# Optimization experiments

Measured on AMD Instinct MI355X. Metric: run time of the kernel, lower is better.

Reference implementation:

```python
import jax, jax.numpy as jnp
import numpy as np

E, TOPK, H, I = 8, 2, 2048, 5632
T = 4096


def setup_inputs() -> dict:
    key = jax.random.key(0)
    k1, k2, k3, k4 = jax.random.split(key, 4)
    hidden_states = jax.random.normal(k1, (T, H), dtype=jnp.float32)
    gate_w = jax.random.normal(k2, (E, H), dtype=jnp.float32) * (1.0 / np.sqrt(H))
    # fused gate+up projection: [E, 2*I, H]
    w13 = jax.random.normal(k3, (E, 2 * I, H), dtype=jnp.float32) * (1.0 / np.sqrt(H))
    # down projection: [E, H, I]
    w2 = jax.random.normal(k4, (E, H, I), dtype=jnp.float32) * (1.0 / np.sqrt(I))
    return {"hidden_states": hidden_states, "gate_w": gate_w, "w13": w13, "w2": w2, "top_k": TOPK}


def reference(hidden_states, gate_w, w13, w2, top_k):
    num_experts = gate_w.shape[0]
    inter = w2.shape[2]
    # router: fp32 gate logits -> softmax -> top-k -> renormalize (FusedMoE renormalize=True)
    logits = hidden_states.astype(jnp.float32) @ gate_w.T          # [T, E]
    probs = jax.nn.softmax(logits, axis=-1)
    vals, idx = jax.lax.top_k(probs, top_k)                        # [T, k]
    vals = vals / jnp.sum(vals, axis=-1, keepdims=True)
    # dense routing weight matrix [T, E] (zero outside top-k)
    dense_w = jnp.sum(jax.nn.one_hot(idx, num_experts, dtype=vals.dtype) * vals[..., None], axis=1)

    def body(acc, inputs):
        w13_e, w2_e, we = inputs                                   # [2I,H], [H,I], [T]
        gu = hidden_states @ w13_e.T                               # [T, 2I]
        g, u = gu[:, :inter], gu[:, inter:]
        h = jax.nn.silu(g) * u                                     # SwiGLU
        y = h @ w2_e.T                                             # [T, H]
        return acc + we[:, None] * y, None

    acc0 = jnp.zeros_like(hidden_states)
    out, _ = jax.lax.scan(body, acc0, (w13, w2, dense_w.T))
    return out
```

## Files before the change

### kernel.cpp

```cpp
#include <hip/hip_runtime.h>

#define T_TOK 4096
#define H_DIM 2048
#define I_DIM 5632
#define NE 8

typedef _Float16 f16;
typedef _Float16 f16x8 __attribute__((ext_vector_type(8)));
typedef float f32x4 __attribute__((ext_vector_type(4)));

#define OFF_META   0
#define OFF_BTOK   256
#define OFF_BW     (256 + 32768)
#define OFF_RE     (256 + 2 * 32768)
#define OFF_RW     (256 + 3 * 32768)
#define OFF_TP     (256 + 4 * 32768)
#define OFF_HSB    (256 + 5 * 32768)
#define OFF_WF     (OFF_HSB + (size_t)T_TOK * H_DIM * 2)

typedef const __attribute__((address_space(1))) unsigned int guint;
typedef __attribute__((address_space(3))) unsigned int luint;

__device__ __forceinline__ int swzk(int r, int bir) {
    return (bir & 15) | ((((bir >> 4) ^ r) & 7) << 4);
}

__global__ void cvt_w_kernel(const float* __restrict__ src, f16* __restrict__ dst, int n8) {
    int stride = gridDim.x * blockDim.x;
    for (int i = blockIdx.x * blockDim.x + threadIdx.x; i < n8; i += stride) {
        size_t b = (size_t)i * 8;
        float4 a = *(const float4*)(src + b);
        float4 c = *(const float4*)(src + b + 4);
        f16x8 v;
        v[0] = (f16)a.x; v[1] = (f16)a.y; v[2] = (f16)a.z; v[3] = (f16)a.w;
        v[4] = (f16)c.x; v[5] = (f16)c.y; v[6] = (f16)c.z; v[7] = (f16)c.w;
        *(f16x8*)(dst + b) = v;
    }
}

__global__ void prep_kernel(const float* __restrict__ w13, f16* __restrict__ w13f, int n8_w13,
                            int cvt13_b,
                            const float* __restrict__ hs, f16* __restrict__ hsb,
                            const float* __restrict__ gw,
                            int* __restrict__ re, float* __restrict__ rw,
                            int* __restrict__ counts) {
    int id = blockIdx.x;
    if (id < cvt13_b) {
        int stride = cvt13_b * 256;
        for (int i = id * 256 + threadIdx.x; i < n8_w13; i += stride) {
            size_t b = (size_t)i * 8;
            float4 a = *(const float4*)(w13 + b);
            float4 c = *(const float4*)(w13 + b + 4);
            f16x8 v;
            v[0] = (f16)a.x; v[1] = (f16)a.y; v[2] = (f16)a.z; v[3] = (f16)a.w;
            v[4] = (f16)c.x; v[5] = (f16)c.y; v[6] = (f16)c.z; v[7] = (f16)c.w;
            *(f16x8*)(w13f + b) = v;
        }
        return;
    }
    id -= cvt13_b;
    if (id < 1024) {
        const int n8 = T_TOK * H_DIM / 8;
        int stride = 1024 * 256;
        for (int i = id * 256 + threadIdx.x; i < n8; i += stride) {
            size_t b = (size_t)i * 8;
            float4 a = *(const float4*)(hs + b);
            float4 c = *(const float4*)(hs + b + 4);
            f16x8 v;
            v[0] = (f16)a.x; v[1] = (f16)a.y; v[2] = (f16)a.z; v[3] = (f16)a.w;
            v[4] = (f16)c.x; v[5] = (f16)c.y; v[6] = (f16)c.z; v[7] = (f16)c.w;
            *(f16x8*)(hsb + b) = v;
        }
        return;
    }
    id -= 1024;
    int lane = threadIdx.x & 63;
    int t = id * 4 + (threadIdx.x >> 6);
    float acc[NE];
#pragma unroll
    for (int e = 0; e < NE; ++e) acc[e] = 0.f;
    const float* x = hs + (size_t)t * H_DIM;
    for (int i = lane; i < H_DIM; i += 64) {
        float xv = x[i];
#pragma unroll
        for (int e = 0; e < NE; ++e) acc[e] += xv * gw[e * H_DIM + i];
    }
#pragma unroll
    for (int e = 0; e < NE; ++e)
        for (int off = 32; off > 0; off >>= 1) acc[e] += __shfl_xor(acc[e], off);
    if (lane == 0) {
        int i1 = 0; float l1 = acc[0];
#pragma unroll
        for (int e = 1; e < NE; ++e) if (acc[e] > l1) { l1 = acc[e]; i1 = e; }
        int i2 = -1; float l2 = -1e30f;
#pragma unroll
        for (int e = 0; e < NE; ++e) if (e != i1 && acc[e] > l2) { l2 = acc[e]; i2 = e; }
        float aa = __expf(l2 - l1);
        float s = 1.f / (1.f + aa);
        re[t * 2] = i1; re[t * 2 + 1] = i2;
        rw[t * 2] = s;  rw[t * 2 + 1] = aa * s;
        atomicAdd(&counts[i1], 1);
        atomicAdd(&counts[i2], 1);
    }
}

__global__ void scan_kernel(int* __restrict__ meta) {
    if (threadIdx.x == 0) {
        int s = 0;
        for (int e = 0; e < NE; ++e) { meta[8 + e] = s; meta[16 + e] = s; s += meta[e]; }
    }
}

__global__ void place_kernel(const int* __restrict__ re, const float* __restrict__ rw,
                             int* __restrict__ cursor, int* __restrict__ btok,
                             float* __restrict__ bwv, int* __restrict__ tpos) {
    int t = blockIdx.x * 256 + threadIdx.x;
    if (t >= T_TOK) return;
#pragma unroll
    for (int s = 0; s < 2; ++s) {
        int e = re[t * 2 + s];
        int p = atomicAdd(&cursor[e], 1);
        btok[p] = t;
        bwv[p] = rw[t * 2 + s];
        tpos[t * 2 + s] = p;
    }
}

__device__ __forceinline__ void decode_panel(int id, int npx, int e_arg,
                                             int& e, int& bx, int& by) {
    if (e_arg >= 0) { e = e_arg; bx = id >> 5; by = id & 31; return; }
    int sg  = id >> 8;
    int rem = id & 255;
    by = rem >> 3;
    int P = sg * 8 + (rem & 7);
    e = P / npx; bx = P % npx;
}

__global__ __launch_bounds__(256, 4) void gemm1_kernel(
    const f16* __restrict__ w13f, const f16* __restrict__ hsb, f16* __restrict__ hb,
    const int* __restrict__ counts, const int* __restrict__ offs,
    const int* __restrict__ btok,
    const float* __restrict__ w2src, f16* __restrict__ w2dst, int cvt_n8, int cvt_blocks,
    int e_arg, int global_h)
{
    if ((int)blockIdx.x < cvt_blocks) {
        int stride = cvt_blocks * 256;
        for (int i = blockIdx.x * 256 + threadIdx.x; i < cvt_n8; i += stride) {
            size_t b = (size_t)i * 8;
            float4 a = *(const float4*)(w2src + b);
            float4 c = *(const float4*)(w2src + b + 4);
            f16x8 v;
            v[0] = (f16)a.x; v[1] = (f16)a.y; v[2] = (f16)a.z; v[3] = (f16)a.w;
            v[4] = (f16)c.x; v[5] = (f16)c.y; v[6] = (f16)c.z; v[7] = (f16)c.w;
            *(f16x8*)(w2dst + b) = v;
        }
        return;
    }
    int e, bx, by;
    decode_panel((int)blockIdx.x - cvt_blocks, 88, e_arg, e, bx, by);
    const int n_e = counts[e];
    if (by * 128 >= n_e) return;
    const int boff = offs[e];
    const f16* We = (e_arg >= 0) ? w13f : (w13f + (size_t)e * (2 * I_DIM) * H_DIM);

    const int tid = threadIdx.x;
    const int lane = tid & 63;
    const int wid = tid >> 6;
    const int wm = wid >> 1, wn = wid & 1;
    const int l15 = lane & 15;

    __shared__ f16 As[128 * 64];
    __shared__ f16 Bs[128 * 64];

    const f16* gA[4]; const f16* gB[4]; int dstc[4];
#pragma unroll
    for (int i = 0; i < 4; ++i) {
        int c = i * 256 + tid;
        int r = c >> 3;
        dstc[i] = c * 16;
        int slot = ((c & 7) ^ (r & 7)) * 8;
        int idx = by * 128 + r;
        idx = idx < n_e ? idx : n_e - 1;
        gA[i] = hsb + (size_t)btok[boff + idx] * H_DIM + slot;
        int wrow = (r < 64) ? (bx * 64 + r) : (I_DIM + bx * 64 + (r - 64));
        gB[i] = We + (size_t)wrow * H_DIM + slot;
    }

    f32x4 ag[4][2], au[4][2];
#pragma unroll
    for (int m = 0; m < 4; ++m)
#pragma unroll
        for (int n = 0; n < 2; ++n) { ag[m][n] = (f32x4)0.f; au[m][n] = (f32x4)0.f; }

    const int NT = H_DIM / 64;

#pragma unroll 1
    for (int kt = 0; kt < NT; ++kt) {
        __syncthreads();
        const int k0 = kt * 64;
#pragma unroll
        for (int i = 0; i < 4; ++i) {
            __builtin_amdgcn_global_load_lds((guint*)(gA[i] + k0), (luint*)((char*)As + dstc[i]), 16, 0, 0);
            __builtin_amdgcn_global_load_lds((guint*)(gB[i] + k0), (luint*)((char*)Bs + dstc[i]), 16, 0, 0);
        }
        __syncthreads();
#pragma unroll
        for (int kh = 0; kh < 2; ++kh) {
            const int kb = kh * 64 + (lane >> 4) * 16;
            f16x8 a[4], bg[2], bu[2];
#pragma unroll
            for (int m = 0; m < 4; ++m) {
                int r = wm * 64 + m * 16 + l15;
                a[m] = *(const f16x8*)((const char*)As + r * 128 + swzk(r, kb));
            }
#pragma unroll
            for (int n = 0; n < 2; ++n) {
                int rg = wn * 32 + n * 16 + l15;
                bg[n] = *(const f16x8*)((const char*)Bs + rg * 128 + swzk(rg, kb));
                int ru = 64 + rg;
                bu[n] = *(const f16x8*)((const char*)Bs + ru * 128 + swzk(ru, kb));
            }
#pragma unroll
            for (int m = 0; m < 4; ++m)
#pragma unroll
                for (int n = 0; n < 2; ++n) {
                    ag[m][n] = __builtin_amdgcn_mfma_f32_16x16x32_f16(a[m], bg[n], ag[m][n], 0, 0, 0);
                    au[m][n] = __builtin_amdgcn_mfma_f32_16x16x32_f16(a[m], bu[n], au[m][n], 0, 0, 0);
                }
        }
    }

    const int hbase = (global_h ? boff : 0) + by * 128;
#pragma unroll
    for (int m = 0; m < 4; ++m) {
        int rl0 = wm * 64 + m * 16 + ((lane >> 4) << 2);
#pragma unroll
        for (int r = 0; r < 4; ++r) {
            int rl = rl0 + r;
            if (by * 128 + rl < n_e) {
#pragma unroll
                for (int n = 0; n < 2; ++n) {
                    float g = ag[m][n][r];
                    float u = au[m][n][r];
                    float h = g / (1.f + __expf(-g)) * u;
                    hb[(size_t)(hbase + rl) * I_DIM + bx * 64 + wn * 32 + n * 16 + l15] = (f16)h;
                }
            }
        }
    }
}

__global__ __launch_bounds__(256, 4) void gemm2_kernel(
    const f16* __restrict__ w2f, const f16* __restrict__ hb, f16* __restrict__ y,
    const int* __restrict__ counts, const int* __restrict__ offs,
    const int* __restrict__ btok, int e_arg, int global_h)
{
    int e, bx, by;
    decode_panel(blockIdx.x, 16, e_arg, e, bx, by);
    const int n_e = counts[e];
    if (by * 128 >= n_e) return;
    const int boff = offs[e];
    const f16* We = (e_arg >= 0) ? w2f : (w2f + (size_t)e * H_DIM * I_DIM);

    const int tid = threadIdx.x;
    const int lane = tid & 63;
    const int wid = tid >> 6;
    const int wm = wid >> 1, wn = wid & 1;
    const int l15 = lane & 15;

    __shared__ f16 As[128 * 64];
    __shared__ f16 Bs[128 * 64];

    const int hb0 = global_h ? boff : 0;
    const f16* gA[4]; const f16* gB[4]; int dstc[4];
#pragma unroll
    for (int i = 0; i < 4; ++i) {
        int c = i * 256 + tid;
        int r = c >> 3;
        dstc[i] = c * 16;
        int slot = ((c & 7) ^ (r & 7)) * 8;
        int idx = by * 128 + r;
        idx = idx < n_e ? idx : n_e - 1;
        gA[i] = hb + (size_t)(hb0 + idx) * I_DIM + slot;
        gB[i] = We + (size_t)(bx * 128 + r) * I_DIM + slot;
    }

    f32x4 acc[4][4];
#pragma unroll
    for (int m = 0; m < 4; ++m)
#pragma unroll
        for (int n = 0; n < 4; ++n) acc[m][n] = (f32x4)0.f;

    const int NT = I_DIM / 64;

#pragma unroll 1
    for (int kt = 0; kt < NT; ++kt) {
        __syncthreads();
        const int k0 = kt * 64;
#pragma unroll
        for (int i = 0; i < 4; ++i) {
            __builtin_amdgcn_global_load_lds((guint*)(gA[i] + k0), (luint*)((char*)As + dstc[i]), 16, 0, 0);
            __builtin_amdgcn_global_load_lds((guint*)(gB[i] + k0), (luint*)((char*)Bs + dstc[i]), 16, 0, 0);
        }
        __syncthreads();
#pragma unroll
        for (int kh = 0; kh < 2; ++kh) {
            const int kb = kh * 64 + (lane >> 4) * 16;
            f16x8 a[4], b[4];
#pragma unroll
            for (int m = 0; m < 4; ++m) {
                int r = wm * 64 + m * 16 + l15;
                a[m] = *(const f16x8*)((const char*)As + r * 128 + swzk(r, kb));
            }
#pragma unroll
            for (int n = 0; n < 4; ++n) {
                int r = wn * 64 + n * 16 + l15;
                b[n] = *(const f16x8*)((const char*)Bs + r * 128 + swzk(r, kb));
            }
#pragma unroll
            for (int m = 0; m < 4; ++m)
#pragma unroll
                for (int n = 0; n < 4; ++n)
                    acc[m][n] = __builtin_amdgcn_mfma_f32_16x16x32_f16(a[m], b[n], acc[m][n], 0, 0, 0);
        }
    }

#pragma unroll
    for (int m = 0; m < 4; ++m) {
        int rl0 = wm * 64 + m * 16 + ((lane >> 4) << 2);
#pragma unroll
        for (int r = 0; r < 4; ++r) {
            int rl = rl0 + r;
            if (by * 128 + rl < n_e) {
                int p = boff + by * 128 + rl;
#pragma unroll
                for (int n = 0; n < 4; ++n)
                    y[(size_t)p * H_DIM + bx * 128 + wn * 64 + n * 16 + l15] = (f16)acc[m][n][r];
            }
        }
    }
}

__global__ void reduce_kernel(const f16* __restrict__ y, const int* __restrict__ tpos,
                              const float* __restrict__ bwv, float* __restrict__ out) {
    int t = blockIdx.x;
    int p0 = tpos[t * 2], p1 = tpos[t * 2 + 1];
    float w0 = bwv[p0], w1 = bwv[p1];
    const f16x8* y0 = (const f16x8*)(y + (size_t)p0 * H_DIM);
    const f16x8* y1 = (const f16x8*)(y + (size_t)p1 * H_DIM);
    float4* o = (float4*)(out + (size_t)t * H_DIM);
    for (int i = threadIdx.x; i < H_DIM / 8; i += 256) {
        f16x8 a = y0[i], b = y1[i];
        float4 r0, r1;
        r0.x = w0 * (float)a[0] + w1 * (float)b[0];
        r0.y = w0 * (float)a[1] + w1 * (float)b[1];
        r0.z = w0 * (float)a[2] + w1 * (float)b[2];
        r0.w = w0 * (float)a[3] + w1 * (float)b[3];
        r1.x = w0 * (float)a[4] + w1 * (float)b[4];
        r1.y = w0 * (float)a[5] + w1 * (float)b[5];
        r1.z = w0 * (float)a[6] + w1 * (float)b[6];
        r1.w = w0 * (float)a[7] + w1 * (float)b[7];
        o[i * 2]     = r0;
        o[i * 2 + 1] = r1;
    }
}

extern "C" void kernel_launch(void* const* d_in, const int* in_sizes, int n_in,
                              void* d_out, int out_size, void* d_ws, size_t ws_size,
                              hipStream_t stream) {
    const float* hs  = (const float*)d_in[0];
    const float* gw  = (const float*)d_in[1];
    const float* w13 = (const float*)d_in[2];
    const float* w2  = (const float*)d_in[3];
    float* out = (float*)d_out;

    char* ws = (char*)d_ws;
    int*   meta = (int*)(ws + OFF_META);
    int*   btok = (int*)(ws + OFF_BTOK);
    float* bwv  = (float*)(ws + OFF_BW);
    int*   re   = (int*)(ws + OFF_RE);
    float* rw   = (float*)(ws + OFF_RW);
    int*   tpos = (int*)(ws + OFF_TP);
    f16*   hsb  = (f16*)(ws + OFF_HSB);

    hipMemsetAsync(meta, 0, 256, stream);

    const size_t w13_elems = (size_t)NE * 2 * I_DIM * H_DIM;
    const size_t w2_elems  = (size_t)NE * H_DIM * I_DIM;

    size_t o_w13f = OFF_WF;
    size_t o_w2f  = o_w13f + w13_elems * 2;
    size_t o_hb   = o_w2f + w2_elems * 2;
    size_t o_y    = o_hb + (size_t)2 * T_TOK * I_DIM * 2;
    size_t need_full = o_y + (size_t)2 * T_TOK * H_DIM * 2;

    size_t f_w13 = OFF_WF;
    size_t f_w2  = f_w13 + (size_t)2 * I_DIM * H_DIM * 2;
    size_t f_hb  = f_w2 + (size_t)H_DIM * I_DIM * 2;
    size_t f_y   = f_hb + (size_t)T_TOK * I_DIM * 2;

    if (ws_size >= need_full) {
        f16* w13f = (f16*)(ws + o_w13f);
        f16* w2f  = (f16*)(ws + o_w2f);
        f16* hb   = (f16*)(ws + o_hb);
        f16* y    = (f16*)(ws + o_y);
        prep_kernel<<<3072 + 1024 + 1024, 256, 0, stream>>>(
            w13, w13f, (int)(w13_elems / 8), 3072, hs, hsb, gw, re, rw, meta);
        scan_kernel<<<1, 64, 0, stream>>>(meta);
        place_kernel<<<T_TOK / 256, 256, 0, stream>>>(re, rw, meta + 16, btok, bwv, tpos);
        gemm1_kernel<<<2048 + 704 * 32, 256, 0, stream>>>(
            w13f, hsb, hb, meta, meta + 8, btok,
            w2, w2f, (int)(w2_elems / 8), 2048, -1, 1);
        gemm2_kernel<<<128 * 32, 256, 0, stream>>>(w2f, hb, y, meta, meta + 8, btok, -1, 1);
        reduce_kernel<<<T_TOK, 256, 0, stream>>>(y, tpos, bwv, out);
    } else {
        f16* w13f = (f16*)(ws + f_w13);
        f16* w2f  = (f16*)(ws + f_w2);
        f16* hb   = (f16*)(ws + f_hb);
        f16* y    = (f16*)(ws + f_y);
        prep_kernel<<<1024 + 1024, 256, 0, stream>>>(
            w13, (f16*)nullptr, 0, 0, hs, hsb, gw, re, rw, meta);
        scan_kernel<<<1, 64, 0, stream>>>(meta);
        place_kernel<<<T_TOK / 256, 256, 0, stream>>>(re, rw, meta + 16, btok, bwv, tpos);
        const size_t w13_slice = (size_t)2 * I_DIM * H_DIM;
        const size_t w2_slice  = (size_t)H_DIM * I_DIM;
        for (int e = 0; e < NE; ++e) {
            cvt_w_kernel<<<2048, 256, 0, stream>>>(w13 + e * w13_slice, w13f, (int)(w13_slice / 8));
            gemm1_kernel<<<2048 + 88 * 32, 256, 0, stream>>>(
                w13f, hsb, hb, meta, meta + 8, btok,
                w2 + e * w2_slice, w2f, (int)(w2_slice / 8), 2048, e, 0);
            gemm2_kernel<<<16 * 32, 256, 0, stream>>>(w2f, hb, y, meta, meta + 8, btok, e, 0);
        }
        reduce_kernel<<<T_TOK, 256, 0, stream>>>(y, tpos, bwv, out);
    }
}
```

Baseline: 1.127 ms.

## Use two-wave blocks with larger per-wave tiles in both MoE GEMMs

```diff
diff --git a/kernel.cpp b/kernel.cpp
--- a/kernel.cpp
+++ b/kernel.cpp
@@ -136,7 +136,7 @@
     e = P / npx; bx = P % npx;
 }
 
-__global__ __launch_bounds__(256, 4) void gemm1_kernel(
+__global__ __launch_bounds__(128, 2) void gemm1_kernel(
     const f16* __restrict__ w13f, const f16* __restrict__ hsb, f16* __restrict__ hb,
     const int* __restrict__ counts, const int* __restrict__ offs,
     const int* __restrict__ btok,
@@ -144,8 +144,8 @@
     int e_arg, int global_h)
 {
     if ((int)blockIdx.x < cvt_blocks) {
-        int stride = cvt_blocks * 256;
-        for (int i = blockIdx.x * 256 + threadIdx.x; i < cvt_n8; i += stride) {
+        int stride = cvt_blocks * 128;
+        for (int i = blockIdx.x * 128 + threadIdx.x; i < cvt_n8; i += stride) {
             size_t b = (size_t)i * 8;
             float4 a = *(const float4*)(w2src + b);
             float4 c = *(const float4*)(w2src + b + 4);
@@ -165,20 +165,18 @@
 
     const int tid = threadIdx.x;
     const int lane = tid & 63;
-    const int wid = tid >> 6;
-    const int wm = wid >> 1, wn = wid & 1;
+    const int wn = tid >> 6;
     const int l15 = lane & 15;
 
     __shared__ f16 As[128 * 64];
     __shared__ f16 Bs[128 * 64];
 
-    const f16* gA[4]; const f16* gB[4]; int dstc[4];
-#pragma unroll
-    for (int i = 0; i < 4; ++i) {
-        int c = i * 256 + tid;
-        int r = c >> 3;
-        dstc[i] = c * 16;
-        int slot = ((c & 7) ^ (r & 7)) * 8;
+    const int r0 = tid >> 3;
+    const int slot = ((tid & 7) ^ (r0 & 7)) * 8;
+    const f16* gA[8]; const f16* gB[8];
+#pragma unroll
+    for (int i = 0; i < 8; ++i) {
+        int r = i * 16 + r0;
         int idx = by * 128 + r;
         idx = idx < n_e ? idx : n_e - 1;
         gA[i] = hsb + (size_t)btok[boff + idx] * H_DIM + slot;
@@ -186,9 +184,9 @@
         gB[i] = We + (size_t)wrow * H_DIM + slot;
     }
 
-    f32x4 ag[4][2], au[4][2];
-#pragma unroll
-    for (int m = 0; m < 4; ++m)
+    f32x4 ag[8][2], au[8][2];
+#pragma unroll
+    for (int m = 0; m < 8; ++m)
 #pragma unroll
         for (int n = 0; n < 2; ++n) { ag[m][n] = (f32x4)0.f; au[m][n] = (f32x4)0.f; }
 
@@ -199,18 +197,20 @@
         __syncthreads();
         const int k0 = kt * 64;
 #pragma unroll
-        for (int i = 0; i < 4; ++i) {
-            __builtin_amdgcn_global_load_lds((guint*)(gA[i] + k0), (luint*)((char*)As + dstc[i]), 16, 0, 0);
-            __builtin_amdgcn_global_load_lds((guint*)(gB[i] + k0), (luint*)((char*)Bs + dstc[i]), 16, 0, 0);
+        for (int i = 0; i < 8; ++i) {
+            __builtin_amdgcn_global_load_lds((guint*)(gA[i] + k0),
+                (luint*)((char*)As + i * 2048 + tid * 16), 16, 0, 0);
+            __builtin_amdgcn_global_load_lds((guint*)(gB[i] + k0),
+                (luint*)((char*)Bs + i * 2048 + tid * 16), 16, 0, 0);
         }
         __syncthreads();
 #pragma unroll
         for (int kh = 0; kh < 2; ++kh) {
             const int kb = kh * 64 + (lane >> 4) * 16;
-            f16x8 a[4], bg[2], bu[2];
-#pragma unroll
-            for (int m = 0; m < 4; ++m) {
-                int r = wm * 64 + m * 16 + l15;
+            f16x8 a[8], bg[2], bu[2];
+#pragma unroll
+            for (int m = 0; m < 8; ++m) {
+                int r = m * 16 + l15;
                 a[m] = *(const f16x8*)((const char*)As + r * 128 + swzk(r, kb));
             }
 #pragma unroll
@@ -221,7 +221,7 @@
                 bu[n] = *(const f16x8*)((const char*)Bs + ru * 128 + swzk(ru, kb));
             }
 #pragma unroll
-            for (int m = 0; m < 4; ++m)
+            for (int m = 0; m < 8; ++m)
 #pragma unroll
                 for (int n = 0; n < 2; ++n) {
                     ag[m][n] = __builtin_amdgcn_mfma_f32_16x16x32_f16(a[m], bg[n], ag[m][n], 0, 0, 0);
@@ -232,8 +232,8 @@
 
     const int hbase = (global_h ? boff : 0) + by * 128;
 #pragma unroll
-    for (int m = 0; m < 4; ++m) {
-        int rl0 = wm * 64 + m * 16 + ((lane >> 4) << 2);
+    for (int m = 0; m < 8; ++m) {
+        int rl0 = m * 16 + ((lane >> 4) << 2);
 #pragma unroll
         for (int r = 0; r < 4; ++r) {
             int rl = rl0 + r;
@@ -250,7 +250,7 @@
     }
 }
 
-__global__ __launch_bounds__(256, 4) void gemm2_kernel(
+__global__ __launch_bounds__(128, 2) void gemm2_kernel(
     const f16* __restrict__ w2f, const f16* __restrict__ hb, f16* __restrict__ y,
     const int* __restrict__ counts, const int* __restrict__ offs,
     const int* __restrict__ btok, int e_arg, int global_h)
@@ -264,30 +264,28 @@
 
     const int tid = threadIdx.x;
     const int lane = tid & 63;
-    const int wid = tid >> 6;
-    const int wm = wid >> 1, wn = wid & 1;
+    const int wn = tid >> 6;
     const int l15 = lane & 15;
 
     __shared__ f16 As[128 * 64];
     __shared__ f16 Bs[128 * 64];
 
     const int hb0 = global_h ? boff : 0;
-    const f16* gA[4]; const f16* gB[4]; int dstc[4];
-#pragma unroll
-    for (int i = 0; i < 4; ++i) {
-        int c = i * 256 + tid;
-        int r = c >> 3;
-        dstc[i] = c * 16;
-        int slot = ((c & 7) ^ (r & 7)) * 8;
+    const int r0 = tid >> 3;
+    const int slot = ((tid & 7) ^ (r0 & 7)) * 8;
+    const f16* gA[8]; const f16* gB[8];
+#pragma unroll
+    for (int i = 0; i < 8; ++i) {
+        int r = i * 16 + r0;
         int idx = by * 128 + r;
         idx = idx < n_e ? idx : n_e - 1;
         gA[i] = hb + (size_t)(hb0 + idx) * I_DIM + slot;
         gB[i] = We + (size_t)(bx * 128 + r) * I_DIM + slot;
     }
 
-    f32x4 acc[4][4];
-#pragma unroll
-    for (int m = 0; m < 4; ++m)
+    f32x4 acc[8][4];
+#pragma unroll
+    for (int m = 0; m < 8; ++m)
 #pragma unroll
         for (int n = 0; n < 4; ++n) acc[m][n] = (f32x4)0.f;
 
@@ -298,18 +296,20 @@
         __syncthreads();
         const int k0 = kt * 64;
 #pragma unroll
-        for (int i = 0; i < 4; ++i) {
-            __builtin_amdgcn_global_load_lds((guint*)(gA[i] + k0), (luint*)((char*)As + dstc[i]), 16, 0, 0);
-            __builtin_amdgcn_global_load_lds((guint*)(gB[i] + k0), (luint*)((char*)Bs + dstc[i]), 16, 0, 0);
+        for (int i = 0; i < 8; ++i) {
+            __builtin_amdgcn_global_load_lds((guint*)(gA[i] + k0),
+                (luint*)((char*)As + i * 2048 + tid * 16), 16, 0, 0);
+            __builtin_amdgcn_global_load_lds((guint*)(gB[i] + k0),
+                (luint*)((char*)Bs + i * 2048 + tid * 16), 16, 0, 0);
         }
         __syncthreads();
 #pragma unroll
         for (int kh = 0; kh < 2; ++kh) {
             const int kb = kh * 64 + (lane >> 4) * 16;
-            f16x8 a[4], b[4];
-#pragma unroll
-            for (int m = 0; m < 4; ++m) {
-                int r = wm * 64 + m * 16 + l15;
+            f16x8 a[8], b[4];
+#pragma unroll
+            for (int m = 0; m < 8; ++m) {
+                int r = m * 16 + l15;
                 a[m] = *(const f16x8*)((const char*)As + r * 128 + swzk(r, kb));
             }
 #pragma unroll
@@ -318,7 +318,7 @@
                 b[n] = *(const f16x8*)((const char*)Bs + r * 128 + swzk(r, kb));
             }
 #pragma unroll
-            for (int m = 0; m < 4; ++m)
+            for (int m = 0; m < 8; ++m)
 #pragma unroll
                 for (int n = 0; n < 4; ++n)
                     acc[m][n] = __builtin_amdgcn_mfma_f32_16x16x32_f16(a[m], b[n], acc[m][n], 0, 0, 0);
@@ -326,8 +326,8 @@
     }
 
 #pragma unroll
-    for (int m = 0; m < 4; ++m) {
-        int rl0 = wm * 64 + m * 16 + ((lane >> 4) << 2);
+    for (int m = 0; m < 8; ++m) {
+        int rl0 = m * 16 + ((lane >> 4) << 2);
 #pragma unroll
         for (int r = 0; r < 4; ++r) {
             int rl = rl0 + r;
@@ -408,10 +408,10 @@
             w13, w13f, (int)(w13_elems / 8), 3072, hs, hsb, gw, re, rw, meta);
         scan_kernel<<<1, 64, 0, stream>>>(meta);
         place_kernel<<<T_TOK / 256, 256, 0, stream>>>(re, rw, meta + 16, btok, bwv, tpos);
-        gemm1_kernel<<<2048 + 704 * 32, 256, 0, stream>>>(
+        gemm1_kernel<<<2048 + 704 * 32, 128, 0, stream>>>(
             w13f, hsb, hb, meta, meta + 8, btok,
             w2, w2f, (int)(w2_elems / 8), 2048, -1, 1);
-        gemm2_kernel<<<128 * 32, 256, 0, stream>>>(w2f, hb, y, meta, meta + 8, btok, -1, 1);
+        gemm2_kernel<<<128 * 32, 128, 0, stream>>>(w2f, hb, y, meta, meta + 8, btok, -1, 1);
         reduce_kernel<<<T_TOK, 256, 0, stream>>>(y, tpos, bwv, out);
     } else {
         f16* w13f = (f16*)(ws + f_w13);
@@ -426,10 +426,10 @@
         const size_t w2_slice  = (size_t)H_DIM * I_DIM;
         for (int e = 0; e < NE; ++e) {
             cvt_w_kernel<<<2048, 256, 0, stream>>>(w13 + e * w13_slice, w13f, (int)(w13_slice / 8));
-            gemm1_kernel<<<2048 + 88 * 32, 256, 0, stream>>>(
+            gemm1_kernel<<<2048 + 88 * 32, 128, 0, stream>>>(
                 w13f, hsb, hb, meta, meta + 8, btok,
                 w2 + e * w2_slice, w2f, (int)(w2_slice / 8), 2048, e, 0);
-            gemm2_kernel<<<16 * 32, 256, 0, stream>>>(w2f, hb, y, meta, meta + 8, btok, e, 0);
+            gemm2_kernel<<<16 * 32, 128, 0, stream>>>(w2f, hb, y, meta, meta + 8, btok, e, 0);
         }
         reduce_kernel<<<T_TOK, 256, 0, stream>>>(y, tpos, bwv, out);
     }
```

Result: slower. 1.179 ms (+4.6%).
